# Performance work log

Hardware: AMD Instinct MI355X
Metric: run time of the kernel (lower is better)

## Reference

```python
import jax, jax.numpy as jnp
import numpy as np

D_STATE = 16
D_CONV = 4
DT_RANK = 16  # ceil(d_model/16) = ceil(256/16)
N_LAYERS = 2
EPS = 1e-5


def _layernorm(x, g, b):
    m = jnp.mean(x, -1, keepdims=True)
    v = jnp.var(x, -1, keepdims=True)
    return (x - m) * jax.lax.rsqrt(v + EPS) * g + b


def _causal_conv(x, w, b):
    # x [B,L,D], depthwise causal conv, w [D,K], b [D]
    K = w.shape[1]
    L = x.shape[1]
    xp = jnp.pad(x, ((0, 0), (K - 1, 0), (0, 0)))
    y = sum(xp[:, k:k + L, :] * w[:, k] for k in range(K))
    return y + b


def _selective_scan(u, dt, A, Bm, Cm, D_skip):
    # u, dt [B,L,d]; A [d,n]; Bm, Cm [B,L,n]; D_skip [d]
    def step(h, inp):
        dt_t, B_t, C_t, u_t = inp  # [B,d],[B,n],[B,n],[B,d]
        dA = jnp.exp(dt_t[:, :, None] * A)                      # [B,d,n]
        h = dA * h + dt_t[:, :, None] * B_t[:, None, :] * u_t[:, :, None]
        y = jnp.einsum('bdn,bn->bd', h, C_t)
        return h, y

    Bsz, L, d = u.shape
    h0 = jnp.zeros((Bsz, d, A.shape[1]), u.dtype)
    xs = (dt.transpose(1, 0, 2), Bm.transpose(1, 0, 2),
          Cm.transpose(1, 0, 2), u.transpose(1, 0, 2))
    _, ys = jax.lax.scan(step, h0, xs)                          # [L,B,d]
    return ys.transpose(1, 0, 2) + u * D_skip


def _mamba_block(x, Wip, cw, cb, Wxp, Wdt, bdt, Alog, Dp, Wout):
    xz = x @ Wip                                                # [B,L,2*d_inner]
    d_inner = Wip.shape[1] // 2
    xc, z = xz[..., :d_inner], xz[..., d_inner:]
    xc = jax.nn.silu(_causal_conv(xc, cw, cb))
    xdbl = xc @ Wxp                                             # [B,L,dt_rank+2n]
    dt = jax.nn.softplus(xdbl[..., :DT_RANK] @ Wdt + bdt)
    Bm = xdbl[..., DT_RANK:DT_RANK + D_STATE]
    Cm = xdbl[..., DT_RANK + D_STATE:]
    A = -jnp.exp(Alog)
    y = _selective_scan(xc, dt, A, Bm, Cm, Dp)
    y = y * jax.nn.silu(z)
    return y @ Wout


def reference(z_t, W_in, b_in, ln_g, ln_b, W_inproj, conv_w, conv_b, W_xproj,
              W_dt, b_dt, A_log, D_skip, W_out, W_outp, b_outp, lno_g, lno_b):
    x = z_t @ W_in + b_in                                       # [B,L,d_model]
    for i in range(N_LAYERS):
        res = x
        xn = _layernorm(x, ln_g[i], ln_b[i])
        x = res + _mamba_block(xn, W_inproj[i], conv_w[i], conv_b[i],
                               W_xproj[i], W_dt[i], b_dt[i], A_log[i],
                               D_skip[i], W_out[i])  # dropout is identity in eval
    u = x @ W_outp + b_outp
    return _layernorm(u, lno_g, lno_b)


def setup_inputs() -> dict:
    key = jax.random.key(0)
    B, L = 16, 2048
    d_input, d_model, d_output, d_inner = 1088, 256, 64, 512
    n = N_LAYERS
    ks = jax.random.split(key, 10)

    def rn(k, shape, fan):
        return jax.random.normal(k, shape, jnp.float32) / np.float32(np.sqrt(fan))

    A_init = jnp.log(jnp.arange(1, D_STATE + 1, dtype=jnp.float32))
    return {
        'z_t': jax.random.normal(ks[0], (B, L, d_input), jnp.float32),
        'W_in': rn(ks[1], (d_input, d_model), d_input),
        'b_in': jnp.zeros((d_model,), jnp.float32),
        'ln_g': jnp.ones((n, d_model), jnp.float32),
        'ln_b': jnp.zeros((n, d_model), jnp.float32),
        'W_inproj': rn(ks[2], (n, d_model, 2 * d_inner), d_model),
        'conv_w': rn(ks[3], (n, d_inner, D_CONV), D_CONV),
        'conv_b': jnp.zeros((n, d_inner), jnp.float32),
        'W_xproj': rn(ks[4], (n, d_inner, DT_RANK + 2 * D_STATE), d_inner),
        'W_dt': rn(ks[5], (n, DT_RANK, d_inner), DT_RANK),
        'b_dt': jnp.full((n, d_inner), -4.6, jnp.float32),  # softplus ~ 0.01
        'A_log': jnp.broadcast_to(A_init, (n, d_inner, D_STATE)) + 0.0,
        'D_skip': jnp.ones((n, d_inner), jnp.float32),
        'W_out': rn(ks[6], (n, d_inner, d_model), d_inner),
        'W_outp': rn(ks[7], (d_model, d_output), d_model),
        'b_outp': jnp.zeros((d_output,), jnp.float32),
        'lno_g': jnp.ones((d_output,), jnp.float32),
        'lno_b': jnp.zeros((d_output,), jnp.float32),
    }
```

## Files before the change

kernel.cpp:

```cpp
#include <hip/hip_runtime.h>
#include <hip/hip_bf16.h>
#include <math.h>
#include <stdint.h>

#define L_SEQ 2048
#define BATCH 16
#define NROWS (BATCH * L_SEQ)
#define DMODEL 256
#define DINNER 512
#define C_CH 32
#define T_CH 64
#define LOG2E 1.4426950408889634f

typedef __attribute__((ext_vector_type(8))) __bf16 bf16x8;
typedef __attribute__((ext_vector_type(4))) float f32x4;
typedef __attribute__((ext_vector_type(8))) unsigned short u16x8;
typedef __attribute__((address_space(1))) const uint32_t gu32;
typedef __attribute__((address_space(3))) uint32_t lu32;

#if __has_builtin(__builtin_amdgcn_exp2f)
#define EXP2F __builtin_amdgcn_exp2f
#else
#define EXP2F exp2f
#endif

__device__ __forceinline__ float sigmoidf_(float x) { return 1.f / (1.f + __expf(-x)); }

__device__ __forceinline__ unsigned short f2bf(float f) {
    union { float f; uint32_t u; } v; v.f = f;
    uint32_t r = v.u + 0x7FFF + ((v.u >> 16) & 1);
    return (unsigned short)(r >> 16);
}
__device__ __forceinline__ float bf2f(unsigned short h) {
    union { uint32_t u; float f; } v; v.u = ((uint32_t)h) << 16;
    return v.f;
}

__device__ __forceinline__ void gld16(const void* g, void* l) {
    __builtin_amdgcn_global_load_lds((gu32*)g, (lu32*)l, 16, 0, 0);
}

template <int N> __device__ __forceinline__ void waitv() {
    if constexpr (N == 0)       asm volatile("s_waitcnt vmcnt(0)" ::: "memory");
    else if constexpr (N == 3)  asm volatile("s_waitcnt vmcnt(3)" ::: "memory");
    else if constexpr (N == 4)  asm volatile("s_waitcnt vmcnt(4)" ::: "memory");
    else if constexpr (N == 5)  asm volatile("s_waitcnt vmcnt(5)" ::: "memory");
    else if constexpr (N == 6)  asm volatile("s_waitcnt vmcnt(6)" ::: "memory");
    else if constexpr (N == 8)  asm volatile("s_waitcnt vmcnt(8)" ::: "memory");
    else if constexpr (N == 10) asm volatile("s_waitcnt vmcnt(10)" ::: "memory");
    else if constexpr (N == 16) asm volatile("s_waitcnt vmcnt(16)" ::: "memory");
}

__global__ __launch_bounds__(256) void wtrans_all(
    const float* __restrict__ W_in, const float* __restrict__ W_inpr,
    const float* __restrict__ W_out, const float* __restrict__ W_xproj,
    const float* __restrict__ W_outp,
    unsigned short* __restrict__ WinT, unsigned short* __restrict__ WipT,
    unsigned short* __restrict__ WoutT, unsigned short* __restrict__ WxpT,
    unsigned short* __restrict__ WopT)
{
    const int bid = blockIdx.x, tid = threadIdx.x;
    if (bid < 1088) {
        int idx = bid * 256 + tid;
        int n = idx / 1088, k = idx % 1088;
        WinT[idx] = f2bf(W_in[(size_t)k * 256 + n]);
    } else if (bid < 3136) {
        int l = (bid - 1088) >> 10;
        int idx = ((bid - 1088) & 1023) * 256 + tid;
        int n = idx >> 8, k = idx & 255;
        WipT[(size_t)l * 262144 + idx] = f2bf(W_inpr[(size_t)l * 262144 + (size_t)k * 1024 + n]);
    } else if (bid < 4160) {
        int l = (bid - 3136) >> 9;
        int idx = ((bid - 3136) & 511) * 256 + tid;
        int n = idx >> 9, k = idx & 511;
        WoutT[(size_t)l * 131072 + idx] = f2bf(W_out[(size_t)l * 131072 + (size_t)k * 256 + n]);
    } else if (bid < 4672) {
        int l = (bid - 4160) >> 8;
        int idx = ((bid - 4160) & 255) * 256 + tid;
        int n = idx >> 9, k = idx & 511;
        WxpT[(size_t)l * 65536 + idx] =
            (n < 48) ? f2bf(W_xproj[(size_t)l * (512 * 48) + (size_t)k * 48 + n]) : (unsigned short)0;
    } else {
        int idx = (bid - 4672) * 256 + tid;
        int n = idx >> 8, k = idx & 255;
        WopT[idx] = (n < 64) ? f2bf(W_outp[(size_t)k * 64 + n]) : (unsigned short)0;
    }
}

template <int TM, int TN, int BK, bool A_F32, bool HAS_BIAS, bool HAS_RES,
          bool OUT_BF16, bool LN64OUT, bool LN256OUT>
__global__ __launch_bounds__(256) void gemm_bf16(
    const void* __restrict__ Aptr, const unsigned short* __restrict__ Bt,
    const float* __restrict__ bias, const float* __restrict__ res,
    void* __restrict__ Cout, int M, int N, int K, int Nout,
    const float* __restrict__ lng, const float* __restrict__ lnb,
    unsigned short* __restrict__ xnout)
{
    constexpr int MR = TM / 32;
    constexpr int NR = TN / 32;
    constexpr int EWA = A_F32 ? 4 : 2;
    constexpr int RBA = BK * EWA;
    constexpr int RBB = BK * 2;
    constexpr int ABYTES = TM * RBA;
    constexpr int BBYTES = TN * RBB;
    constexpr int OPSA = ABYTES / 4096;
    constexpr int OPSB = BBYTES / 4096;
    constexpr int VOPS = OPSA + OPSB;
    constexpr bool SWZA = (RBA >= 128);
    constexpr bool SWZB = (RBB >= 128);
    constexpr int KK = BK / 32;
    __shared__ __align__(16) char Alds[2][ABYTES];
    __shared__ __align__(16) char Blds[2][BBYTES];
    const int tid = threadIdx.x;
    const int w = tid >> 6, lane = tid & 63;

    const int nwg = gridDim.x;
    const int q = nwg >> 3;
    const int wg = (blockIdx.x & 7) * q + (blockIdx.x >> 3);
    const int nx = N / TN;
    const int bm = (wg / nx) * TM, bn = (wg % nx) * TN;

    const int wr = (w >> 1) * (TM / 2), wc = (w & 1) * (TN / 2);
    const int fr = lane & 15, fq = lane >> 4;
    const size_t KbB = (size_t)K * 2;
    const size_t KbA = (size_t)K * EWA;

    const char* Ab = (const char*)Aptr;
    const char* Bb = (const char*)Bt;
    const int lds0 = w * 1024;

    f32x4 acc[MR][NR];
#pragma unroll
    for (int m = 0; m < MR; m++)
#pragma unroll
        for (int n = 0; n < NR; n++) acc[m][n] = (f32x4){0.f, 0.f, 0.f, 0.f};

    auto stageA = [&](int buf, int k0) {
        char* lA = Alds[buf];
#pragma unroll
        for (int i = 0; i < OPSA; i++) {
            const int o = i * 4096 + tid * 16;
            const int row = o / RBA;
            int col = o % RBA;
            if constexpr (SWZA) col ^= (row & 7) << 4;
            gld16(Ab + (size_t)(bm + row) * KbA + (size_t)k0 * EWA + col,
                  lA + i * 4096 + lds0);
        }
    };
    auto stageB = [&](int buf, int k0) {
        char* lB = Blds[buf];
#pragma unroll
        for (int i = 0; i < OPSB; i++) {
            const int o = i * 4096 + tid * 16;
            const int row = o / RBB;
            int col = o % RBB;
            if constexpr (SWZB) col ^= (row & 7) << 4;
            gld16(Bb + (size_t)(bn + row) * KbB + (size_t)k0 * 2 + col,
                  lB + i * 4096 + lds0);
        }
    };
    auto compute = [&](int buf) {
        const char* lA = Alds[buf];
        const char* lB = Blds[buf];
#pragma unroll
        for (int kk = 0; kk < KK; kk++) {
            bf16x8 af[MR], bg[NR];
#pragma unroll
            for (int m = 0; m < MR; m++) {
                const int row = wr + m * 16 + fr;
                const int sw = SWZA ? ((row & 7) << 4) : 0;
                if constexpr (A_F32) {
                    const int b0 = row * RBA + kk * 128 + fq * 32;
                    float4 x0 = *(const float4*)(lA + (b0 ^ sw));
                    float4 x1 = *(const float4*)(lA + ((b0 + 16) ^ sw));
                    bf16x8 a;
                    a[0]=(__bf16)x0.x; a[1]=(__bf16)x0.y; a[2]=(__bf16)x0.z; a[3]=(__bf16)x0.w;
                    a[4]=(__bf16)x1.x; a[5]=(__bf16)x1.y; a[6]=(__bf16)x1.z; a[7]=(__bf16)x1.w;
                    af[m] = a;
                } else {
                    const int c = kk * 64 + fq * 16;
                    af[m] = *(const bf16x8*)(lA + row * RBA + (c ^ sw));
                }
            }
#pragma unroll
            for (int n = 0; n < NR; n++) {
                const int row = wc + n * 16 + fr;
                const int sw = SWZB ? ((row & 7) << 4) : 0;
                const int c = kk * 64 + fq * 16;
                bg[n] = *(const bf16x8*)(lB + row * RBB + (c ^ sw));
            }
#pragma unroll
            for (int m = 0; m < MR; m++)
#pragma unroll
                for (int n = 0; n < NR; n++)
                    acc[m][n] = __builtin_amdgcn_mfma_f32_16x16x32_bf16(af[m], bg[n], acc[m][n], 0, 0, 0);
        }
    };

    const int NT = K / BK;

    stageA(0, 0); stageB(0, 0);
    asm volatile("s_waitcnt vmcnt(0) lgkmcnt(0)" ::: "memory");
    __builtin_amdgcn_s_barrier();
    __builtin_amdgcn_sched_barrier(0);

    for (int kt = 0; kt < NT; ++kt) {
        const int cur = kt & 1;
        const bool has_next = (kt + 1 < NT);
        if (has_next) {
            const int k0 = (kt + 1) * BK;
            stageA(cur ^ 1, k0); stageB(cur ^ 1, k0);
            waitv<VOPS>();
        } else {
            waitv<0>();
        }
        __builtin_amdgcn_s_barrier();
        __builtin_amdgcn_sched_barrier(0);

        compute(cur);

        asm volatile("s_waitcnt lgkmcnt(0)" ::: "memory");
        __builtin_amdgcn_s_barrier();
        __builtin_amdgcn_sched_barrier(0);
    }

    if constexpr (LN256OUT) {
        float* xout = (float*)Cout;
        float s_[MR][4], sq_[MR][4];
#pragma unroll
        for (int m = 0; m < MR; m++)
#pragma unroll
            for (int r = 0; r < 4; r++) { s_[m][r] = 0.f; sq_[m][r] = 0.f; }
#pragma unroll
        for (int m = 0; m < MR; m++) {
#pragma unroll
            for (int n = 0; n < NR; n++) {
                const int col = wc + n * 16 + fr;
#pragma unroll
                for (int r = 0; r < 4; r++) {
                    const int row = bm + wr + m * 16 + fq * 4 + r;
                    float v = acc[m][n][r];
                    if (HAS_BIAS) v += bias[col];
                    if (HAS_RES)  v += res[(size_t)row * 256 + col];
                    acc[m][n][r] = v;
                    xout[(size_t)row * 256 + col] = v;
                    s_[m][r] += v; sq_[m][r] += v * v;
                }
            }
        }
#pragma unroll
        for (int m = 0; m < MR; m++)
#pragma unroll
            for (int r = 0; r < 4; r++)
#pragma unroll
                for (int off = 8; off; off >>= 1) {
                    s_[m][r] += __shfl_xor(s_[m][r], off);
                    sq_[m][r] += __shfl_xor(sq_[m][r], off);
                }
        float2* red = (float2*)&Alds[0][0];
        if (fr == 0) {
#pragma unroll
            for (int m = 0; m < MR; m++)
#pragma unroll
                for (int r = 0; r < 4; r++)
                    red[w * 32 + m * 16 + fq * 4 + r] = make_float2(s_[m][r], sq_[m][r]);
        }
        __syncthreads();
#pragma unroll
        for (int m = 0; m < MR; m++) {
#pragma unroll
            for (int r = 0; r < 4; r++) {
                float2 o = red[(w ^ 1) * 32 + m * 16 + fq * 4 + r];
                float s = s_[m][r] + o.x, sq = sq_[m][r] + o.y;
                float mean = s * (1.f / 256.f);
                float var = sq * (1.f / 256.f) - mean * mean;
                float rs = rsqrtf(var + 1e-5f);
                const int row = bm + wr + m * 16 + fq * 4 + r;
#pragma unroll
                for (int n = 0; n < NR; n++) {
                    const int col = wc + n * 16 + fr;
                    xnout[(size_t)row * 256 + col] =
                        f2bf((acc[m][n][r] - mean) * rs * lng[col] + lnb[col]);
                }
            }
        }
    } else if constexpr (LN64OUT) {
        if (wc == 0) {
#pragma unroll
            for (int m = 0; m < MR; m++) {
#pragma unroll
                for (int r = 0; r < 4; r++) {
                    float v[NR]; float s = 0.f, sq = 0.f;
#pragma unroll
                    for (int n = 0; n < NR; n++) {
                        v[n] = acc[m][n][r] + bias[n * 16 + fr];
                        s += v[n]; sq += v[n] * v[n];
                    }
#pragma unroll
                    for (int off = 8; off; off >>= 1) { s += __shfl_xor(s, off); sq += __shfl_xor(sq, off); }
                    float mean = s * (1.f / 64.f);
                    float var = sq * (1.f / 64.f) - mean * mean;
                    float rs = rsqrtf(var + 1e-5f);
                    int row = bm + wr + m * 16 + fq * 4 + r;
#pragma unroll
                    for (int n = 0; n < NR; n++) {
                        int col = n * 16 + fr;
                        ((float*)Cout)[(size_t)row * 64 + col] = (v[n] - mean) * rs * lng[col] + lnb[col];
                    }
                }
            }
        }
    } else {
#pragma unroll
        for (int m = 0; m < MR; m++) {
#pragma unroll
            for (int n = 0; n < NR; n++) {
                int col = bn + wc + n * 16 + fr;
                if (col < Nout) {
#pragma unroll
                    for (int r = 0; r < 4; r++) {
                        int row = bm + wr + m * 16 + fq * 4 + r;
                        float v = acc[m][n][r];
                        if (HAS_BIAS) v += bias[col];
                        if (HAS_RES)  v += res[(size_t)row * Nout + col];
                        if (OUT_BF16) ((unsigned short*)Cout)[(size_t)row * Nout + col] = f2bf(v);
                        else          ((float*)Cout)[(size_t)row * Nout + col] = v;
                    }
                }
            }
        }
    }
}

__global__ __launch_bounds__(256) void conv_silu8(
    const unsigned short* __restrict__ xz, const float* __restrict__ w,
    const float* __restrict__ cb, unsigned short* __restrict__ xc)
{
    int idx = blockIdx.x * 256 + threadIdx.x;
    int d8 = (idx & 63) << 3;
    int l  = (idx >> 6) & 2047;
    int b  = idx >> 17;
    const unsigned short* base = xz + ((size_t)b * L_SEQ + l) * 1024 + d8;
    u16x8 t0 = {0,0,0,0,0,0,0,0}, t1 = t0, t2 = t0;
    u16x8 t3 = *(const u16x8*)base;
    if (l >= 1) t2 = *(const u16x8*)(base - 1024);
    if (l >= 2) t1 = *(const u16x8*)(base - 2048);
    if (l >= 3) t0 = *(const u16x8*)(base - 3072);
    u16x8 o;
#pragma unroll
    for (int j = 0; j < 8; j++) {
        float4 wv = *(const float4*)&w[(d8 + j) * 4];
        float acc = cb[d8 + j];
        acc = fmaf(bf2f(t0[j]), wv.x, acc);
        acc = fmaf(bf2f(t1[j]), wv.y, acc);
        acc = fmaf(bf2f(t2[j]), wv.z, acc);
        acc = fmaf(bf2f(t3[j]), wv.w, acc);
        o[j] = f2bf(acc * sigmoidf_(acc));
    }
    *(u16x8*)&xc[((size_t)b * L_SEQ + l) * 512 + d8] = o;
}

__global__ __launch_bounds__(256) void scan_pass1(
    const unsigned short* __restrict__ xc, const float* __restrict__ xdbl,
    const float* __restrict__ Wdt, const float* __restrict__ bdt,
    const float* __restrict__ Alog,
    float* __restrict__ Tbuf, float* __restrict__ Sbuf)
{
    __shared__ float xs[T_CH][32];
    int idx = blockIdx.x * 256 + threadIdx.x;
    int d = idx & 511;
    int c = (idx >> 9) & (C_CH - 1);
    int b = idx >> 14;
    size_t r0 = (size_t)b * L_SEQ + (size_t)c * T_CH;
#pragma unroll
    for (int ii = 0; ii < 2; ii++) {
        int i = threadIdx.x + ii * 256, row = i >> 3, qq = i & 7;
        *(float4*)&xs[row][qq * 4] = *(const float4*)&xdbl[(r0 + row) * 48 + qq * 4];
    }
    __syncthreads();

    float wdt[16];
#pragma unroll
    for (int j = 0; j < 16; j++) wdt[j] = Wdt[j * 512 + d];
    const float bd = bdt[d];

    float a[16], a2[16], S[16];
#pragma unroll
    for (int n = 0; n < 16; n++) a[n] = -__expf(Alog[d * 16 + n]);
#pragma unroll
    for (int n = 0; n < 16; n++) a2[n] = a[n] * LOG2E;
#pragma unroll
    for (int n = 0; n < 16; n++) S[n] = 0.f;
    bool pow_ok = true;
#pragma unroll
    for (int n = 1; n < 16; n++)
        pow_ok = pow_ok && (fabsf(a[n] - (n + 1) * a[0]) <= 1e-3f * (n + 1) * fabsf(a[0]));
    const float a0l2 = a[0] * LOG2E;
    float Tsum = 0.f;

    if (pow_ok) {
        for (int t = 0; t < T_CH; t++) {
            float dtr = bd;
#pragma unroll
            for (int j = 0; j < 16; j++) dtr = fmaf(xs[t][j], wdt[j], dtr);
            float dtv = (dtr > 20.f) ? dtr : __logf(1.f + __expf(dtr));
            float u = bf2f(xc[(r0 + t) * 512 + d]);
            float dtu = dtv * u;
            Tsum += dtv;
            float e1 = EXP2F(dtv * a0l2), e2 = e1 * e1;
            S[0] = fmaf(e1, S[0], dtu * xs[t][16]);
            S[1] = fmaf(e2, S[1], dtu * xs[t][17]);
            float pm2 = e1, pm1 = e2;
#pragma unroll
            for (int n = 2; n < 16; n++) {
                float cur = pm2 * e2;
                S[n] = fmaf(cur, S[n], dtu * xs[t][16 + n]);
                pm2 = pm1; pm1 = cur;
            }
        }
    } else {
        for (int t = 0; t < T_CH; t++) {
            float dtr = bd;
#pragma unroll
            for (int j = 0; j < 16; j++) dtr = fmaf(xs[t][j], wdt[j], dtr);
            float dtv = (dtr > 20.f) ? dtr : __logf(1.f + __expf(dtr));
            float u = bf2f(xc[(r0 + t) * 512 + d]);
            float dtu = dtv * u;
            Tsum += dtv;
#pragma unroll
            for (int n = 0; n < 16; n++) {
                float dA = EXP2F(dtv * a2[n]);
                S[n] = fmaf(dA, S[n], dtu * xs[t][16 + n]);
            }
        }
    }
    Tbuf[idx] = Tsum;
    size_t o = (size_t)idx * 16;
#pragma unroll
    for (int qq = 0; qq < 4; qq++)
        *(float4*)&Sbuf[o + qq * 4] = make_float4(S[qq*4], S[qq*4+1], S[qq*4+2], S[qq*4+3]);
}

__global__ __launch_bounds__(256) void scan_pass2(
    const float* __restrict__ Tbuf, const float* __restrict__ Alog,
    float* __restrict__ Sbuf)
{
    int g = blockIdx.x * 256 + threadIdx.x;
    int nd = g & 8191;
    int b = g >> 13;
    int d = nd >> 4, n = nd & 15;
    const float a2 = -__expf(Alog[d * 16 + n]) * LOG2E;
    float H = 0.f;
    for (int c = 0; c < C_CH; c++) {
        size_t base = (size_t)(b * C_CH + c);
        float T = Tbuf[base * 512 + d];
        float P = EXP2F(T * a2);
        size_t idx = base * 8192 + nd;
        float S = Sbuf[idx];
        float Hn = fmaf(P, H, S);
        Sbuf[idx] = H;
        H = Hn;
    }
}

__global__ __launch_bounds__(256) void scan_pass3(
    const unsigned short* __restrict__ xcin, const unsigned short* __restrict__ xz,
    const float* __restrict__ xdbl, const float* __restrict__ Wdt,
    const float* __restrict__ bdt, const float* __restrict__ Alog,
    const float* __restrict__ Dsk, const float* __restrict__ Sbuf,
    unsigned short* __restrict__ y)
{
    __shared__ float xs[T_CH][48];
    int idx = blockIdx.x * 256 + threadIdx.x;
    int d = idx & 511;
    int c = (idx >> 9) & (C_CH - 1);
    int b = idx >> 14;
    size_t r0 = (size_t)b * L_SEQ + (size_t)c * T_CH;
#pragma unroll
    for (int ii = 0; ii < 3; ii++) {
        int i = threadIdx.x + ii * 256, row = i / 12, qq = i % 12;
        *(float4*)&xs[row][qq * 4] = *(const float4*)&xdbl[(r0 + row) * 48 + qq * 4];
    }
    __syncthreads();

    float wdt[16];
#pragma unroll
    for (int j = 0; j < 16; j++) wdt[j] = Wdt[j * 512 + d];
    const float bd = bdt[d];

    float a[16], a2[16], h[16];
#pragma unroll
    for (int n = 0; n < 16; n++) a[n] = -__expf(Alog[d * 16 + n]);
#pragma unroll
    for (int n = 0; n < 16; n++) a2[n] = a[n] * LOG2E;
    {
        size_t o = (size_t)idx * 16;
#pragma unroll
        for (int qq = 0; qq < 4; qq++) {
            float4 v = *(const float4*)&Sbuf[o + qq * 4];
            h[qq*4] = v.x; h[qq*4+1] = v.y; h[qq*4+2] = v.z; h[qq*4+3] = v.w;
        }
    }
    bool pow_ok = true;
#pragma unroll
    for (int n = 1; n < 16; n++)
        pow_ok = pow_ok && (fabsf(a[n] - (n + 1) * a[0]) <= 1e-3f * (n + 1) * fabsf(a[0]));
    const float a0l2 = a[0] * LOG2E;
    const float Dv = Dsk[d];

    if (pow_ok) {
        for (int t = 0; t < T_CH; t++) {
            size_t ridx = (r0 + t) * 512 + d;
            float dtr = bd;
#pragma unroll
            for (int j = 0; j < 16; j++) dtr = fmaf(xs[t][j], wdt[j], dtr);
            float dtv = (dtr > 20.f) ? dtr : __logf(1.f + __expf(dtr));
            float u = bf2f(xcin[ridx]);
            float dtu = dtv * u;
            float e1 = EXP2F(dtv * a0l2), e2 = e1 * e1;
            float yv = 0.f;
            h[0] = fmaf(e1, h[0], dtu * xs[t][16]);  yv = fmaf(h[0], xs[t][32], yv);
            h[1] = fmaf(e2, h[1], dtu * xs[t][17]);  yv = fmaf(h[1], xs[t][33], yv);
            float pm2 = e1, pm1 = e2;
#pragma unroll
            for (int n = 2; n < 16; n++) {
                float cur = pm2 * e2;
                h[n] = fmaf(cur, h[n], dtu * xs[t][16 + n]);
                yv = fmaf(h[n], xs[t][32 + n], yv);
                pm2 = pm1; pm1 = cur;
            }
            yv = fmaf(u, Dv, yv);
            float z = bf2f(xz[(r0 + t) * 1024 + 512 + d]);
            y[ridx] = f2bf(yv * z * sigmoidf_(z));
        }
    } else {
        for (int t = 0; t < T_CH; t++) {
            size_t ridx = (r0 + t) * 512 + d;
            float dtr = bd;
#pragma unroll
            for (int j = 0; j < 16; j++) dtr = fmaf(xs[t][j], wdt[j], dtr);
            float dtv = (dtr > 20.f) ? dtr : __logf(1.f + __expf(dtr));
            float u = bf2f(xcin[ridx]);
            float dtu = dtv * u;
            float yv = 0.f;
#pragma unroll
            for (int n = 0; n < 16; n++) {
                float dA = EXP2F(dtv * a2[n]);
                h[n] = fmaf(dA, h[n], dtu * xs[t][16 + n]);
                yv = fmaf(h[n], xs[t][32 + n], yv);
            }
            yv = fmaf(u, Dv, yv);
            float z = bf2f(xz[(r0 + t) * 1024 + 512 + d]);
            y[ridx] = f2bf(yv * z * sigmoidf_(z));
        }
    }
}

extern "C" void kernel_launch(void* const* d_in, const int* in_sizes, int n_in,
                              void* d_out, int out_size, void* d_ws, size_t ws_size,
                              hipStream_t stream)
{
    const float* z_t     = (const float*)d_in[0];
    const float* W_in    = (const float*)d_in[1];
    const float* b_in    = (const float*)d_in[2];
    const float* ln_g    = (const float*)d_in[3];
    const float* ln_b    = (const float*)d_in[4];
    const float* W_inpr  = (const float*)d_in[5];
    const float* conv_w  = (const float*)d_in[6];
    const float* conv_b  = (const float*)d_in[7];
    const float* W_xproj = (const float*)d_in[8];
    const float* W_dt    = (const float*)d_in[9];
    const float* b_dt    = (const float*)d_in[10];
    const float* A_log   = (const float*)d_in[11];
    const float* D_skip  = (const float*)d_in[12];
    const float* W_out   = (const float*)d_in[13];
    const float* W_outp  = (const float*)d_in[14];
    const float* b_outp  = (const float*)d_in[15];
    const float* lno_g   = (const float*)d_in[16];
    const float* lno_b   = (const float*)d_in[17];
    float* out           = (float*)d_out;

    char* p = (char*)d_ws;
    float*          x    = (float*)p;          p += (size_t)NROWS * DMODEL * 4;
    unsigned short* xn   = (unsigned short*)p; p += (size_t)NROWS * DMODEL * 2;
    unsigned short* xc   = (unsigned short*)p; p += (size_t)NROWS * DINNER * 2;
    unsigned short* xz   = (unsigned short*)p; p += (size_t)NROWS * 1024 * 2;
    float*          xdbl = (float*)p;          p += (size_t)NROWS * 48 * 4;
    float*          Pregion = (float*)p;       p += (size_t)BATCH * C_CH * DINNER * 16 * 4;
    float*          Sbuf = (float*)p;          p += (size_t)BATCH * C_CH * DINNER * 16 * 4;
    unsigned short* WinT  = (unsigned short*)p; p += (size_t)256 * 1088 * 2;
    unsigned short* WipT  = (unsigned short*)p; p += (size_t)2 * 1024 * 256 * 2;
    unsigned short* WoutT = (unsigned short*)p; p += (size_t)2 * 256 * 512 * 2;
    unsigned short* WxpT  = (unsigned short*)p; p += (size_t)2 * 128 * 512 * 2;
    unsigned short* WopT  = (unsigned short*)p; p += (size_t)128 * 256 * 2;
    float* Tbuf = Pregion;

    wtrans_all<<<4800, 256, 0, stream>>>(W_in, W_inpr, W_out, W_xproj, W_outp,
                                         WinT, WipT, WoutT, WxpT, WopT);

    gemm_bf16<64, 256, 32, true, true, false, false, false, true><<<NROWS / 64, 256, 0, stream>>>(
        z_t, WinT, b_in, nullptr, x, NROWS, 256, 1088, 256, ln_g, ln_b, xn);

    for (int layer = 0; layer < 2; ++layer) {
        gemm_bf16<128, 128, 64, false, false, false, true, false, false><<<(NROWS / 128) * (1024 / 128), 256, 0, stream>>>(
            xn, WipT + (size_t)layer * 1024 * 256, nullptr, nullptr, xz, NROWS, 1024, 256, 1024,
            nullptr, nullptr, nullptr);
        conv_silu8<<<NROWS * 64 / 256, 256, 0, stream>>>(
            xz, conv_w + layer * 512 * 4, conv_b + layer * 512, xc);
        gemm_bf16<64, 128, 64, false, false, false, false, false, false><<<(NROWS / 64) * (128 / 128), 256, 0, stream>>>(
            xc, WxpT + (size_t)layer * 128 * 512, nullptr, nullptr, xdbl, NROWS, 128, 512, 48,
            nullptr, nullptr, nullptr);

        const float* Al_l  = A_log + layer * 512 * 16;
        const float* Wdt_l = W_dt + layer * 16 * 512;
        const float* bdt_l = b_dt + layer * 512;
        scan_pass1<<<BATCH * C_CH * DINNER / 256, 256, 0, stream>>>(
            xc, xdbl, Wdt_l, bdt_l, Al_l, Tbuf, Sbuf);
        scan_pass2<<<BATCH * DINNER * 16 / 256, 256, 0, stream>>>(Tbuf, Al_l, Sbuf);
        scan_pass3<<<BATCH * C_CH * DINNER / 256, 256, 0, stream>>>(
            xc, xz, xdbl, Wdt_l, bdt_l, Al_l, D_skip + layer * 512, Sbuf, xc);

        if (layer == 0) {
            gemm_bf16<64, 256, 32, false, false, true, false, false, true><<<NROWS / 64, 256, 0, stream>>>(
                xc, WoutT, nullptr, x, x, NROWS, 256, 512, 256, ln_g + 256, ln_b + 256, xn);
        } else {
            gemm_bf16<64, 128, 64, false, false, true, true, false, false><<<(NROWS / 64) * (256 / 128), 256, 0, stream>>>(
                xc, WoutT + (size_t)256 * 512, nullptr, x, xn, NROWS, 256, 512, 256,
                nullptr, nullptr, nullptr);
        }
    }

    gemm_bf16<64, 128, 64, false, true, false, false, true, false><<<(NROWS / 64) * (128 / 128), 256, 0, stream>>>(
        xn, WopT, b_outp, nullptr, out, NROWS, 128, 256, 64, lno_g, lno_b, nullptr);
}
```

Baseline: 510.2 us.

## Stage fp32 A through registers as bf16 and split input GEMM from layernorm

The first GEMM (fp32 input) now loads A into registers, converts it to bf16 and writes bf16 to LDS, instead of staging fp32 in LDS and converting on every fragment read. This halves A's LDS footprint and removes the repeated conversion work. The tile changes from 64x256/BK32 to 64x128/BK64, giving more workgroups. The fused layernorm epilogue is replaced by a separate ln256 kernel, which adds an extra pass over x in exchange for a simpler GEMM and more parallelism.

```diff
diff --git a/kernel.cpp b/kernel.cpp
--- a/kernel.cpp
+++ b/kernel.cpp
@@ -96,16 +96,15 @@
     const float* __restrict__ lng, const float* __restrict__ lnb,
     unsigned short* __restrict__ xnout)
 {
+    static_assert(!A_F32 || (TM == 64 && BK == 64), "A_F32 reg-staging assumes TM=64,BK=64");
     constexpr int MR = TM / 32;
     constexpr int NR = TN / 32;
-    constexpr int EWA = A_F32 ? 4 : 2;
-    constexpr int RBA = BK * EWA;
+    constexpr int RBA = BK * 2;
     constexpr int RBB = BK * 2;
     constexpr int ABYTES = TM * RBA;
     constexpr int BBYTES = TN * RBB;
     constexpr int OPSA = ABYTES / 4096;
     constexpr int OPSB = BBYTES / 4096;
-    constexpr int VOPS = OPSA + OPSB;
     constexpr bool SWZA = (RBA >= 128);
     constexpr bool SWZB = (RBB >= 128);
     constexpr int KK = BK / 32;
@@ -123,7 +122,7 @@
     const int wr = (w >> 1) * (TM / 2), wc = (w & 1) * (TN / 2);
     const int fr = lane & 15, fq = lane >> 4;
     const size_t KbB = (size_t)K * 2;
-    const size_t KbA = (size_t)K * EWA;
+    const size_t KbA = (size_t)K * (A_F32 ? 4 : 2);
 
     const char* Ab = (const char*)Aptr;
     const char* Bb = (const char*)Bt;
@@ -135,6 +134,27 @@
 #pragma unroll
         for (int n = 0; n < NR; n++) acc[m][n] = (f32x4){0.f, 0.f, 0.f, 0.f};
 
+    float4 ra0, ra1, ra2, ra3;
+    auto loadA = [&](int k0) {
+        const char* src = Ab + (size_t)(bm + (tid >> 2)) * KbA + (size_t)k0 * 4 + (tid & 3) * 64;
+        ra0 = *(const float4*)(src);
+        ra1 = *(const float4*)(src + 16);
+        ra2 = *(const float4*)(src + 32);
+        ra3 = *(const float4*)(src + 48);
+    };
+    auto writeA = [&](int buf) {
+        const int row = tid >> 2;
+        const int sw = SWZA ? ((row & 7) << 4) : 0;
+        const int base = row * RBA + (tid & 3) * 32;
+        char* lA = Alds[buf];
+        bf16x8 v0, v1;
+        v0[0]=(__bf16)ra0.x; v0[1]=(__bf16)ra0.y; v0[2]=(__bf16)ra0.z; v0[3]=(__bf16)ra0.w;
+        v0[4]=(__bf16)ra1.x; v0[5]=(__bf16)ra1.y; v0[6]=(__bf16)ra1.z; v0[7]=(__bf16)ra1.w;
+        v1[0]=(__bf16)ra2.x; v1[1]=(__bf16)ra2.y; v1[2]=(__bf16)ra2.z; v1[3]=(__bf16)ra2.w;
+        v1[4]=(__bf16)ra3.x; v1[5]=(__bf16)ra3.y; v1[6]=(__bf16)ra3.z; v1[7]=(__bf16)ra3.w;
+        *(bf16x8*)(lA + (base ^ sw)) = v0;
+        *(bf16x8*)(lA + ((base + 16) ^ sw)) = v1;
+    };
     auto stageA = [&](int buf, int k0) {
         char* lA = Alds[buf];
 #pragma unroll
@@ -143,7 +163,7 @@
             const int row = o / RBA;
             int col = o % RBA;
             if constexpr (SWZA) col ^= (row & 7) << 4;
-            gld16(Ab + (size_t)(bm + row) * KbA + (size_t)k0 * EWA + col,
+            gld16(Ab + (size_t)(bm + row) * KbA + (size_t)k0 * 2 + col,
                   lA + i * 4096 + lds0);
         }
     };
@@ -169,18 +189,8 @@
             for (int m = 0; m < MR; m++) {
                 const int row = wr + m * 16 + fr;
                 const int sw = SWZA ? ((row & 7) << 4) : 0;
-                if constexpr (A_F32) {
-                    const int b0 = row * RBA + kk * 128 + fq * 32;
-                    float4 x0 = *(const float4*)(lA + (b0 ^ sw));
-                    float4 x1 = *(const float4*)(lA + ((b0 + 16) ^ sw));
-                    bf16x8 a;
-                    a[0]=(__bf16)x0.x; a[1]=(__bf16)x0.y; a[2]=(__bf16)x0.z; a[3]=(__bf16)x0.w;
-                    a[4]=(__bf16)x1.x; a[5]=(__bf16)x1.y; a[6]=(__bf16)x1.z; a[7]=(__bf16)x1.w;
-                    af[m] = a;
-                } else {
-                    const int c = kk * 64 + fq * 16;
-                    af[m] = *(const bf16x8*)(lA + row * RBA + (c ^ sw));
-                }
+                const int c = kk * 64 + fq * 16;
+                af[m] = *(const bf16x8*)(lA + row * RBA + (c ^ sw));
             }
 #pragma unroll
             for (int n = 0; n < NR; n++) {
@@ -199,29 +209,62 @@
 
     const int NT = K / BK;
 
-    stageA(0, 0); stageB(0, 0);
-    asm volatile("s_waitcnt vmcnt(0) lgkmcnt(0)" ::: "memory");
-    __builtin_amdgcn_s_barrier();
-    __builtin_amdgcn_sched_barrier(0);
-
-    for (int kt = 0; kt < NT; ++kt) {
-        const int cur = kt & 1;
-        const bool has_next = (kt + 1 < NT);
-        if (has_next) {
-            const int k0 = (kt + 1) * BK;
-            stageA(cur ^ 1, k0); stageB(cur ^ 1, k0);
-            waitv<VOPS>();
-        } else {
-            waitv<0>();
-        }
-        __builtin_amdgcn_s_barrier();
-        __builtin_amdgcn_sched_barrier(0);
-
-        compute(cur);
-
+    if constexpr (A_F32) {
+        loadA(0); stageB(0, 0);
+        asm volatile("s_waitcnt vmcnt(0)" ::: "memory");
+        writeA(0);
         asm volatile("s_waitcnt lgkmcnt(0)" ::: "memory");
         __builtin_amdgcn_s_barrier();
         __builtin_amdgcn_sched_barrier(0);
+
+        for (int kt = 0; kt < NT; ++kt) {
+            const int cur = kt & 1;
+            const bool has_next = (kt + 1 < NT);
+            if (has_next) {
+                const int k0 = (kt + 1) * BK;
+                loadA(k0); stageB(cur ^ 1, k0);
+                waitv<4 + OPSB>();
+            } else {
+                waitv<0>();
+            }
+            __builtin_amdgcn_s_barrier();
+            __builtin_amdgcn_sched_barrier(0);
+
+            compute(cur);
+
+            if (has_next) {
+                waitv<OPSB>();
+                writeA(cur ^ 1);
+            }
+            asm volatile("s_waitcnt lgkmcnt(0)" ::: "memory");
+            __builtin_amdgcn_s_barrier();
+            __builtin_amdgcn_sched_barrier(0);
+        }
+    } else {
+        stageA(0, 0); stageB(0, 0);
+        asm volatile("s_waitcnt vmcnt(0) lgkmcnt(0)" ::: "memory");
+        __builtin_amdgcn_s_barrier();
+        __builtin_amdgcn_sched_barrier(0);
+
+        for (int kt = 0; kt < NT; ++kt) {
+            const int cur = kt & 1;
+            const bool has_next = (kt + 1 < NT);
+            if (has_next) {
+                const int k0 = (kt + 1) * BK;
+                stageA(cur ^ 1, k0); stageB(cur ^ 1, k0);
+                waitv<OPSA + OPSB>();
+            } else {
+                waitv<0>();
+            }
+            __builtin_amdgcn_s_barrier();
+            __builtin_amdgcn_sched_barrier(0);
+
+            compute(cur);
+
+            asm volatile("s_waitcnt lgkmcnt(0)" ::: "memory");
+            __builtin_amdgcn_s_barrier();
+            __builtin_amdgcn_sched_barrier(0);
+        }
     }
 
     if constexpr (LN256OUT) {
@@ -330,6 +373,30 @@
             }
         }
     }
+}
+
+__global__ __launch_bounds__(256) void ln256(
+    const float* __restrict__ x, const float* __restrict__ g,
+    const float* __restrict__ b, unsigned short* __restrict__ out)
+{
+    int lane = threadIdx.x & 63, wid = threadIdx.x >> 6;
+    size_t r = (size_t)blockIdx.x * 4 + wid;
+    const float4 v = *(const float4*)&x[r * 256 + lane * 4];
+    float s = v.x + v.y + v.z + v.w;
+    float sq = v.x * v.x + v.y * v.y + v.z * v.z + v.w * v.w;
+#pragma unroll
+    for (int off = 32; off; off >>= 1) { s += __shfl_xor(s, off); sq += __shfl_xor(sq, off); }
+    float mean = s * (1.f / 256.f);
+    float var = sq * (1.f / 256.f) - mean * mean;
+    float rs = rsqrtf(var + 1e-5f);
+    float4 gv = *(const float4*)&g[lane * 4];
+    float4 bv = *(const float4*)&b[lane * 4];
+    ushort4 o;
+    o.x = f2bf((v.x - mean) * rs * gv.x + bv.x);
+    o.y = f2bf((v.y - mean) * rs * gv.y + bv.y);
+    o.z = f2bf((v.z - mean) * rs * gv.z + bv.z);
+    o.w = f2bf((v.w - mean) * rs * gv.w + bv.w);
+    *(ushort4*)&out[r * 256 + lane * 4] = o;
 }
 
 __global__ __launch_bounds__(256) void conv_silu8(
@@ -598,8 +665,9 @@
     wtrans_all<<<4800, 256, 0, stream>>>(W_in, W_inpr, W_out, W_xproj, W_outp,
                                          WinT, WipT, WoutT, WxpT, WopT);
 
-    gemm_bf16<64, 256, 32, true, true, false, false, false, true><<<NROWS / 64, 256, 0, stream>>>(
-        z_t, WinT, b_in, nullptr, x, NROWS, 256, 1088, 256, ln_g, ln_b, xn);
+    gemm_bf16<64, 128, 64, true, true, false, false, false, false><<<(NROWS / 64) * (256 / 128), 256, 0, stream>>>(
+        z_t, WinT, b_in, nullptr, x, NROWS, 256, 1088, 256, nullptr, nullptr, nullptr);
+    ln256<<<NROWS / 4, 256, 0, stream>>>(x, ln_g, ln_b, xn);
 
     for (int layer = 0; layer < 2; ++layer) {
         gemm_bf16<128, 128, 64, false, false, false, true, false, false><<<(NROWS / 128) * (1024 / 128), 256, 0, stream>>>(
```

After: 535.2 us. 4.9% more time.
